# Optimization experiments

Measured on AMD Instinct MI355X. Metric: run time of the kernel, lower is better.

The kernel has to match this reference:

```python
import jax, jax.numpy as jnp
import numpy as np

N_HEAD = 16
D_HEAD = 64
D_MODEL = 1024
D_INNER = 4096
QLEN = 1024
MLEN = 1024
BSZ = 2
LN_EPS = 1e-5


def _layer_norm(x, g, b, eps=LN_EPS):
    mu = jnp.mean(x, axis=-1, keepdims=True)
    var = jnp.var(x, axis=-1, keepdims=True)
    return (x - mu) * jax.lax.rsqrt(var + eps) * g + b


def _rel_shift(x):
    # x: [qlen, rlen, bsz, n_head]
    q, r, b, n = x.shape
    zp = jnp.zeros((q, 1, b, n), x.dtype)
    xp = jnp.concatenate([zp, x], axis=1).reshape(r + 1, q, b, n)
    return xp[1:].reshape(q, r, b, n)


def setup_inputs() -> dict:
    key = jax.random.key(0)
    ks = jax.random.split(key, 12)
    klen = MLEN + QLEN
    w = jax.random.normal(ks[0], (QLEN, BSZ, D_MODEL), jnp.float32)
    r = jax.random.normal(ks[1], (klen, D_MODEL), jnp.float32)
    mems = jax.random.normal(ks[2], (MLEN, BSZ, D_MODEL), jnp.float32)
    # causal mask: query i attends keys j <= i + mlen
    i = jnp.arange(QLEN)[:, None]
    j = jnp.arange(klen)[None, :]
    attn_mask = (j > i + MLEN)[:, :, None]  # [qlen, klen, 1] bool
    s = 0.02
    params = dict(
        qkv_w=jax.random.normal(ks[3], (3 * N_HEAD * D_HEAD, D_MODEL), jnp.float32) * s,
        r_net_w=jax.random.normal(ks[4], (N_HEAD * D_HEAD, D_MODEL), jnp.float32) * s,
        o_w=jax.random.normal(ks[5], (D_MODEL, N_HEAD * D_HEAD), jnp.float32) * s,
        r_r_bias=jax.random.normal(ks[6], (N_HEAD, D_HEAD), jnp.float32) * s,
        r_w_bias=jax.random.normal(ks[7], (N_HEAD, D_HEAD), jnp.float32) * s,
        ln1_g=jnp.ones((D_MODEL,), jnp.float32),
        ln1_b=jnp.zeros((D_MODEL,), jnp.float32),
        ff_w1=jax.random.normal(ks[8], (D_INNER, D_MODEL), jnp.float32) * s,
        ff_b1=jnp.zeros((D_INNER,), jnp.float32),
        ff_w2=jax.random.normal(ks[9], (D_MODEL, D_INNER), jnp.float32) * s,
        ff_b2=jnp.zeros((D_MODEL,), jnp.float32),
        ln2_g=jnp.ones((D_MODEL,), jnp.float32),
        ln2_b=jnp.zeros((D_MODEL,), jnp.float32),
    )
    return dict(w=w, r=r, mems=mems, attn_mask=attn_mask, **params)


def reference(w, r, mems, attn_mask, qkv_w, r_net_w, o_w, r_r_bias, r_w_bias,
              ln1_g, ln1_b, ff_w1, ff_b1, ff_w2, ff_b2, ln2_g, ln2_b):
    qlen, bsz = w.shape[0], w.shape[1]
    scale = 1.0 / (D_HEAD ** 0.5)
    cat = jnp.concatenate([mems, w], axis=0)              # [klen, b, d_model]
    klen = cat.shape[0]
    w_heads = cat @ qkv_w.T                                # [klen, b, 3*n*d]
    wq, wk, wv = jnp.split(w_heads, 3, axis=-1)
    wq = wq[-qlen:]
    r_head_k = (r @ r_net_w.T).reshape(-1, N_HEAD, D_HEAD)  # [rlen, n, d]
    wq = wq.reshape(qlen, bsz, N_HEAD, D_HEAD)
    wk = wk.reshape(klen, bsz, N_HEAD, D_HEAD)
    wv = wv.reshape(klen, bsz, N_HEAD, D_HEAD)
    AC = jnp.einsum('ibnd,jbnd->ijbn', wq + r_w_bias, wk)   # content term
    BD = jnp.einsum('ibnd,jnd->ijbn', wq + r_r_bias, r_head_k)
    BD = _rel_shift(BD)                                     # position term
    attn_score = (AC + BD) * scale
    mask_value = jnp.finfo(attn_score.dtype).min
    attn_score = jnp.where(attn_mask[:, :, :, None], mask_value, attn_score)
    attn_prob = jax.nn.softmax(attn_score, axis=1)
    attn_vec = jnp.einsum('ijbn,jbnd->ibnd', attn_prob, wv)
    attn_vec = attn_vec.reshape(qlen, bsz, N_HEAD * D_HEAD)
    attn_out = attn_vec @ o_w.T
    h = _layer_norm(w + attn_out, ln1_g, ln1_b)             # post-lnorm
    core = jax.nn.relu(h @ ff_w1.T + ff_b1) @ ff_w2.T + ff_b2
    out = _layer_norm(h + core, ln2_g, ln2_b)
    return out
```

## Files before the change

### kernel.cpp

```cpp
#include <hip/hip_runtime.h>
#include <math.h>

#define QLEN 1024
#define MLEN 1024
#define KLEN 2048
#define BSZc 2
#define NH 16
#define DH 64
#define DM 1024
#define DI 4096

typedef unsigned short ushort_t;
typedef __attribute__((ext_vector_type(8))) short short8;
typedef __attribute__((ext_vector_type(4))) float f32x4;

__device__ __forceinline__ ushort_t f2bf(float x) {
    unsigned int u = __float_as_uint(x);
    unsigned int r = (u + 0x7FFFu + ((u >> 16) & 1u)) >> 16;
    return (ushort_t)r;
}

__device__ __forceinline__ void gload_lds16(const ushort_t* g, ushort_t* l) {
    __builtin_amdgcn_global_load_lds(
        (const __attribute__((address_space(1))) unsigned int*)g,
        (__attribute__((address_space(3))) unsigned int*)l,
        16, 0, 0);
}

__device__ __forceinline__ void cast8(const float* s, ushort_t* d, int g) {
    const float4 a = *(const float4*)(s + g * 8);
    const float4 b = *(const float4*)(s + g * 8 + 4);
    short8 o;
    o[0] = (short)f2bf(a.x); o[1] = (short)f2bf(a.y);
    o[2] = (short)f2bf(a.z); o[3] = (short)f2bf(a.w);
    o[4] = (short)f2bf(b.x); o[5] = (short)f2bf(b.y);
    o[6] = (short)f2bf(b.z); o[7] = (short)f2bf(b.w);
    *(short8*)(d + g * 8) = o;
}

__global__ __launch_bounds__(256)
void cast_phase1(const float* __restrict__ qkv_w, const float* __restrict__ rnet_w,
                 const float* __restrict__ mems, const float* __restrict__ w,
                 const float* __restrict__ r,
                 ushort_t* __restrict__ W1, ushort_t* __restrict__ W2,
                 ushort_t* __restrict__ Acat, ushort_t* __restrict__ Rsrc)
{
    int g = blockIdx.x * 256 + threadIdx.x;
    if (g < 393216)            { cast8(qkv_w,  W1,              g); }
    else if (g < 524288)       { cast8(rnet_w, W2,              g - 393216); }
    else if (g < 786432)       { cast8(mems,   Acat,            g - 524288); }
    else if (g < 1048576)      { cast8(w,      Acat + 2097152,  g - 786432); }
    else if (g < 1310720)      { cast8(r,      Rsrc,            g - 1048576); }
}

__global__ __launch_bounds__(256)
void cast_phase2(const float* __restrict__ o_w, const float* __restrict__ ffw1,
                 const float* __restrict__ ffw2,
                 ushort_t* __restrict__ W3, ushort_t* __restrict__ W4,
                 ushort_t* __restrict__ W5)
{
    int g = blockIdx.x * 256 + threadIdx.x;
    if (g < 131072)            { cast8(o_w,  W3, g); }
    else if (g < 655360)       { cast8(ffw1, W4, g - 131072); }
    else if (g < 1179648)      { cast8(ffw2, W5, g - 655360); }
}

template<int EMODE, int ACT, int BN>
__global__ __launch_bounds__(256)
void gemm_mfma(const ushort_t* __restrict__ A, const ushort_t* __restrict__ B,
               const float* __restrict__ bias,
               void* __restrict__ O0, int M, int N, int K)
{
    constexpr int JT = BN / 32;
    __shared__ ushort_t At[128 * 32];
    __shared__ ushort_t Bt[BN * 32];

    const int tid  = threadIdx.x;
    const int lane = tid & 63;
    const int w    = tid >> 6;
    const int lr   = lane & 15;
    const int quad = lane >> 4;
    const int m0   = blockIdx.x * 128;
    const int n0   = blockIdx.y * BN;
    const int wm0  = (w >> 1) * 64;
    const int wn0  = (w & 1) * (BN / 2);

    f32x4 acc[4][JT];
#pragma unroll
    for (int it = 0; it < 4; ++it)
#pragma unroll
        for (int jt = 0; jt < JT; ++jt) acc[it][jt] = (f32x4){0.f, 0.f, 0.f, 0.f};

    const int srow = lane >> 2;
    const int scol = (lane & 3) << 3;
    const ushort_t* Ag = A + (size_t)(m0 + w * 32 + srow) * K + scol;
    ushort_t* lA0 = At + (w * 32) * 32;
    ushort_t* lA1 = At + (w * 32 + 16) * 32;
    const ushort_t* Bg;
    ushort_t *lB0, *lB1 = nullptr;
    if (BN == 128) {
        Bg  = B + (size_t)(n0 + w * 32 + srow) * K + scol;
        lB0 = Bt + (w * 32) * 32;
        lB1 = Bt + (w * 32 + 16) * 32;
    } else {
        Bg  = B + (size_t)(n0 + w * 16 + srow) * K + scol;
        lB0 = Bt + (w * 16) * 32;
    }

    const ushort_t* Ato = At + (wm0 + lr) * 32 + quad * 8;
    const ushort_t* Bto = Bt + (wn0 + lr) * 32 + quad * 8;

    for (int k0 = 0; k0 < K; k0 += 32) {
        __syncthreads();
        gload_lds16(Ag + k0, lA0);
        gload_lds16(Ag + (size_t)16 * K + k0, lA1);
        gload_lds16(Bg + k0, lB0);
        if (BN == 128) gload_lds16(Bg + (size_t)16 * K + k0, lB1);
        __syncthreads();

        short8 af[4], bf[JT];
#pragma unroll
        for (int it = 0; it < 4; ++it)
            af[it] = *(const short8*)(Ato + it * 16 * 32);
#pragma unroll
        for (int jt = 0; jt < JT; ++jt)
            bf[jt] = *(const short8*)(Bto + jt * 16 * 32);
#pragma unroll
        for (int it = 0; it < 4; ++it)
#pragma unroll
            for (int jt = 0; jt < JT; ++jt)
                acc[it][jt] = __builtin_amdgcn_mfma_f32_16x16x32_bf16(
                    af[it], bf[jt], acc[it][jt], 0, 0, 0);
    }

#pragma unroll
    for (int it = 0; it < 4; ++it)
#pragma unroll
        for (int jt = 0; jt < JT; ++jt)
#pragma unroll
            for (int rg = 0; rg < 4; ++rg) {
                const int m = m0 + wm0 + it * 16 + quad * 4 + rg;
                const int n = n0 + wn0 + jt * 16 + lr;
                float v = acc[it][jt][rg];
                if (EMODE == 0) {
                    if (bias) v += bias[n];
                    ((float*)O0)[(size_t)m * N + n] = v;
                } else {
                    v += bias[n];
                    if (ACT == 1) v = fmaxf(v, 0.f);
                    ((ushort_t*)O0)[(size_t)m * N + n] = f2bf(v);
                }
            }
}

__global__ __launch_bounds__(256)
void gemm_qkvr(const ushort_t* __restrict__ Acat, const ushort_t* __restrict__ W1,
               const ushort_t* __restrict__ Rsrc, const ushort_t* __restrict__ W2,
               ushort_t* __restrict__ Qac, ushort_t* __restrict__ Qbd,
               ushort_t* __restrict__ Kbf, ushort_t* __restrict__ Vtb,
               ushort_t* __restrict__ Rh,
               const float* __restrict__ rwb, const float* __restrict__ rrb)
{
    __shared__ ushort_t At[128 * 32];
    __shared__ ushort_t Bt[128 * 32];

    const int bid  = blockIdx.x;
    const bool isr = bid >= 768;
    const ushort_t* A; const ushort_t* B; int m0, n0;
    if (!isr) { A = Acat; B = W1; m0 = (bid & 31) * 128; n0 = (bid >> 5) * 128; }
    else { int t = bid - 768; A = Rsrc; B = W2; m0 = (t & 15) * 128; n0 = (t >> 4) * 128; }
    const int K = 1024;

    const int tid  = threadIdx.x;
    const int lane = tid & 63;
    const int w    = tid >> 6;
    const int lr   = lane & 15;
    const int quad = lane >> 4;
    const int wm0  = (w >> 1) * 64;
    const int wn0  = (w & 1) * 64;

    f32x4 acc[4][4];
#pragma unroll
    for (int it = 0; it < 4; ++it)
#pragma unroll
        for (int jt = 0; jt < 4; ++jt) acc[it][jt] = (f32x4){0.f, 0.f, 0.f, 0.f};

    const int srow = lane >> 2;
    const int scol = (lane & 3) << 3;
    const ushort_t* Ag = A + (size_t)(m0 + w * 32 + srow) * K + scol;
    const ushort_t* Bg = B + (size_t)(n0 + w * 32 + srow) * K + scol;
    ushort_t* lA0 = At + (w * 32) * 32;
    ushort_t* lA1 = At + (w * 32 + 16) * 32;
    ushort_t* lB0 = Bt + (w * 32) * 32;
    ushort_t* lB1 = Bt + (w * 32 + 16) * 32;

    const ushort_t* Ato = At + (wm0 + lr) * 32 + quad * 8;
    const ushort_t* Bto = Bt + (wn0 + lr) * 32 + quad * 8;

    for (int k0 = 0; k0 < K; k0 += 32) {
        __syncthreads();
        gload_lds16(Ag + k0, lA0);
        gload_lds16(Ag + (size_t)16 * K + k0, lA1);
        gload_lds16(Bg + k0, lB0);
        gload_lds16(Bg + (size_t)16 * K + k0, lB1);
        __syncthreads();

        short8 af[4], bf[4];
#pragma unroll
        for (int it = 0; it < 4; ++it)
            af[it] = *(const short8*)(Ato + it * 16 * 32);
#pragma unroll
        for (int jt = 0; jt < 4; ++jt)
            bf[jt] = *(const short8*)(Bto + jt * 16 * 32);
#pragma unroll
        for (int it = 0; it < 4; ++it)
#pragma unroll
            for (int jt = 0; jt < 4; ++jt)
                acc[it][jt] = __builtin_amdgcn_mfma_f32_16x16x32_bf16(
                    af[it], bf[jt], acc[it][jt], 0, 0, 0);
    }

#pragma unroll
    for (int it = 0; it < 4; ++it)
#pragma unroll
        for (int jt = 0; jt < 4; ++jt)
#pragma unroll
            for (int rg = 0; rg < 4; ++rg) {
                const int m = m0 + wm0 + it * 16 + quad * 4 + rg;
                const int n = n0 + wn0 + jt * 16 + lr;
                const float v = acc[it][jt][rg];
                if (!isr) {
                    const int j = m >> 1, b = m & 1;
                    const int part = n >> 10, hh = (n >> 6) & 15, d = n & 63;
                    if (part == 0) {
                        if (j >= MLEN) {
                            const int qi = j - MLEN;
                            const size_t qidx = (((size_t)(b * NH + hh)) * QLEN + qi) * DH + d;
                            Qac[qidx] = f2bf(v + rwb[hh * DH + d]);
                            Qbd[qidx] = f2bf(v + rrb[hh * DH + d]);
                        }
                    } else if (part == 1) {
                        Kbf[(((size_t)(b * NH + hh)) * KLEN + j) * DH + d] = f2bf(v);
                    } else {
                        Vtb[(((size_t)(b * NH + hh)) * DH + d) * KLEN + j] = f2bf(v);
                    }
                } else {
                    const int hh = n >> 6, d = n & 63;
                    Rh[(((size_t)hh) * KLEN + m) * DH + d] = f2bf(v);
                }
            }
}

__global__ __launch_bounds__(256)
void attn_mfma(const ushort_t* __restrict__ Qac, const ushort_t* __restrict__ Qbd,
               const ushort_t* __restrict__ Kb, const ushort_t* __restrict__ Vt,
               const ushort_t* __restrict__ Rb,
               float* __restrict__ Op0, float* __restrict__ Op1,
               float* __restrict__ Mp, float* __restrict__ Lp)
{
    __shared__ ushort_t Kt[64][72];
    __shared__ ushort_t Rt[128][72];
    __shared__ ushort_t Vl[64][72];
    __shared__ float    Bw[4][16][84];

    const int tid  = threadIdx.x;
    const int lane = tid & 63;
    const int w    = tid >> 6;
    const int lr   = lane & 15;
    const int quad = lane >> 4;
    const int qt   = blockIdx.x;
    const int s    = blockIdx.y;
    const int bh   = blockIdx.z;
    const int i0   = qt << 6;
    const int h    = bh & 15;
    const int b    = bh >> 4;

    short8 qaf[2], qbf[2];
    {
        const size_t rowoff = ((size_t)bh * QLEN + i0 + w * 16 + lr) * DH;
#pragma unroll
        for (int kt = 0; kt < 2; ++kt) {
            qaf[kt] = *(const short8*)(Qac + rowoff + kt * 32 + quad * 8);
            qbf[kt] = *(const short8*)(Qbd + rowoff + kt * 32 + quad * 8);
        }
    }

    f32x4 O[4];
#pragma unroll
    for (int nt = 0; nt < 4; ++nt) O[nt] = (f32x4){0.f, 0.f, 0.f, 0.f};
    float m_run = -3.4e38f, l_run = 0.f;

    const int nc  = qt + 17;
    const int stw = 3 - w;
    const float SC = 0.125f * 1.44269504f;
    const ushort_t* Kh = Kb + (size_t)bh * KLEN * DH;
    const ushort_t* Vh = Vt + (size_t)bh * DH * KLEN;
    const ushort_t* Rhp = Rb + (size_t)h * KLEN * DH;

    for (int c = s; c < nc; c += 2) {
        const int j0 = c << 6;
        const int wb = 960 - i0 + j0;
        __syncthreads();
#pragma unroll
        for (int t = 0; t < 2; ++t) {
            int f = tid + (t << 8);
            int row = f >> 3, c8 = (f & 7) << 3;
            *(int4*)&Kt[row][c8] = *(const int4*)(Kh + (size_t)(j0 + row) * DH + c8);
        }
#pragma unroll
        for (int t = 0; t < 2; ++t) {
            int f = tid + (t << 8);
            int d = f >> 3, c8 = (f & 7) << 3;
            *(int4*)&Vl[d][c8] = *(const int4*)(Vh + (size_t)d * KLEN + j0 + c8);
        }
#pragma unroll
        for (int t = 0; t < 4; ++t) {
            int f = tid + (t << 8);
            int rl2 = f >> 3, c8 = (f & 7) << 3;
            int g = wb + rl2;
            int gc = g > (KLEN - 1) ? (KLEN - 1) : g;
            *(int4*)&Rt[rl2][c8] = *(const int4*)(Rhp + (size_t)gc * DH + c8);
        }
        __syncthreads();

#pragma unroll
        for (int ctl = 0; ctl < 5; ++ctl) {
            const int wr = (stw + ctl) * 16 + lr;
            f32x4 z = (f32x4){0.f, 0.f, 0.f, 0.f};
#pragma unroll
            for (int kt = 0; kt < 2; ++kt) {
                short8 rb2 = *(const short8*)&Rt[wr][kt * 32 + quad * 8];
                z = __builtin_amdgcn_mfma_f32_16x16x32_bf16(qbf[kt], rb2, z, 0, 0, 0);
            }
#pragma unroll
            for (int rg = 0; rg < 4; ++rg)
                Bw[w][quad * 4 + rg][ctl * 16 + lr] = z[rg];
        }
#pragma unroll
        for (int ct = 0; ct < 4; ++ct) {
            f32x4 z = (f32x4){0.f, 0.f, 0.f, 0.f};
#pragma unroll
            for (int kt = 0; kt < 2; ++kt) {
                short8 kb2 = *(const short8*)&Kt[ct * 16 + lr][kt * 32 + quad * 8];
                z = __builtin_amdgcn_mfma_f32_16x16x32_bf16(qaf[kt], kb2, z, 0, 0, 0);
            }
#pragma unroll
            for (int rg = 0; rg < 4; ++rg) {
                const int rrow = quad * 4 + rg;
                Bw[w][rrow][ct * 16 + lr + 15 - rrow] += z[rg];
            }
        }

        const int lim = i0 + w * 16 + lr + 1024 - j0;
        float pv[16];
        float mx = -3.4e38f;
#pragma unroll
        for (int kt = 0; kt < 2; ++kt)
#pragma unroll
            for (int t = 0; t < 8; ++t) {
                const int jj = kt * 32 + quad * 8 + t;
                float sv = Bw[w][lr][jj + 15 - lr] * SC;
                sv = (jj > lim) ? -3.4e38f : sv;
                pv[kt * 8 + t] = sv;
                mx = fmaxf(mx, sv);
            }
        mx = fmaxf(mx, __shfl_xor(mx, 16, 64));
        mx = fmaxf(mx, __shfl_xor(mx, 32, 64));
        const float m_new = fmaxf(m_run, mx);
        float ps = 0.f;
        short8 pf[2];
#pragma unroll
        for (int kt = 0; kt < 2; ++kt)
#pragma unroll
            for (int t = 0; t < 8; ++t) {
                const float e = exp2f(pv[kt * 8 + t] - m_new);
                ps += e;
                pf[kt][t] = (short)f2bf(e);
            }
        ps += __shfl_xor(ps, 16, 64);
        ps += __shfl_xor(ps, 32, 64);
        const float alpha = exp2f(m_run - m_new);
        m_run = m_new;
        l_run = l_run * alpha + ps;

        float ar[4];
#pragma unroll
        for (int rg = 0; rg < 4; ++rg)
            ar[rg] = __shfl(alpha, quad * 4 + rg, 64);
#pragma unroll
        for (int nt = 0; nt < 4; ++nt) {
            O[nt][0] *= ar[0]; O[nt][1] *= ar[1];
            O[nt][2] *= ar[2]; O[nt][3] *= ar[3];
        }
#pragma unroll
        for (int kt = 0; kt < 2; ++kt)
#pragma unroll
            for (int nt = 0; nt < 4; ++nt) {
                short8 vb = *(const short8*)&Vl[nt * 16 + lr][kt * 32 + quad * 8];
                O[nt] = __builtin_amdgcn_mfma_f32_16x16x32_bf16(pf[kt], vb, O[nt], 0, 0, 0);
            }
    }

    if (quad == 0) {
        const size_t mi = ((size_t)s * 32 + bh) * QLEN + i0 + w * 16 + lr;
        Mp[mi] = m_run;
        Lp[mi] = l_run;
    }
    float* Op = s ? Op1 : Op0;
#pragma unroll
    for (int nt = 0; nt < 4; ++nt)
#pragma unroll
        for (int rg = 0; rg < 4; ++rg) {
            const int i = i0 + w * 16 + quad * 4 + rg;
            Op[((size_t)i * BSZc + b) * DM + h * DH + nt * 16 + lr] = O[nt][rg];
        }
}

__global__ __launch_bounds__(256)
void attn_merge(const float* __restrict__ O0, const float* __restrict__ O1,
                const float* __restrict__ Mp, const float* __restrict__ Lp,
                ushort_t* __restrict__ AV)
{
    const int row = blockIdx.x;
    const int tid = threadIdx.x;
    const int i = row >> 1, b = row & 1;
    const int h = tid >> 4;
    const int bh = b * NH + h;
    const size_t mi = (size_t)bh * QLEN + i;
    const float m1 = Mp[mi],            l1 = Lp[mi];
    const float m2 = Mp[32 * QLEN + mi], l2 = Lp[32 * QLEN + mi];
    const float M = fmaxf(m1, m2);
    const float a1 = exp2f(m1 - M), a2 = exp2f(m2 - M);
    const float rl = 1.f / (l1 * a1 + l2 * a2);
    const float f1 = a1 * rl, f2 = a2 * rl;
    const float4 o1 = ((const float4*)(O0 + (size_t)row * DM))[tid];
    const float4 o2 = ((const float4*)(O1 + (size_t)row * DM))[tid];
    ushort_t* p = AV + (size_t)row * DM + tid * 4;
    p[0] = f2bf(o1.x * f1 + o2.x * f2);
    p[1] = f2bf(o1.y * f1 + o2.y * f2);
    p[2] = f2bf(o1.z * f1 + o2.z * f2);
    p[3] = f2bf(o1.w * f1 + o2.w * f2);
}

__global__ __launch_bounds__(256)
void add_ln(const float* __restrict__ X, const float* __restrict__ Y,
            const float* __restrict__ gg, const float* __restrict__ bb,
            float* __restrict__ out, ushort_t* __restrict__ outb)
{
    const int row  = blockIdx.x;
    const int tid  = threadIdx.x;
    const int lane = tid & 63;
    const int w    = tid >> 6;
    __shared__ float ssum[4], ssq[4];

    const float4 xv = ((const float4*)(X + (size_t)row * DM))[tid];
    const float4 yv = ((const float4*)(Y + (size_t)row * DM))[tid];
    const float v0 = xv.x + yv.x, v1 = xv.y + yv.y;
    const float v2 = xv.z + yv.z, v3 = xv.w + yv.w;
    float s = v0 + v1 + v2 + v3;
    float q = v0 * v0 + v1 * v1 + v2 * v2 + v3 * v3;
#pragma unroll
    for (int off = 32; off > 0; off >>= 1) {
        s += __shfl_xor(s, off, 64);
        q += __shfl_xor(q, off, 64);
    }
    if (lane == 0) { ssum[w] = s; ssq[w] = q; }
    __syncthreads();
    s = ssum[0] + ssum[1] + ssum[2] + ssum[3];
    q = ssq[0] + ssq[1] + ssq[2] + ssq[3];
    const float mean = s * (1.f / DM);
    const float var  = q * (1.f / DM) - mean * mean;
    const float rs   = rsqrtf(var + 1e-5f);
    const float4 g4 = ((const float4*)gg)[tid];
    const float4 b4 = ((const float4*)bb)[tid];
    float4 ov;
    ov.x = (v0 - mean) * rs * g4.x + b4.x;
    ov.y = (v1 - mean) * rs * g4.y + b4.y;
    ov.z = (v2 - mean) * rs * g4.z + b4.z;
    ov.w = (v3 - mean) * rs * g4.w + b4.w;
    ((float4*)(out + (size_t)row * DM))[tid] = ov;
    if (outb) {
        ushort_t* p = outb + (size_t)row * DM + tid * 4;
        p[0] = f2bf(ov.x); p[1] = f2bf(ov.y);
        p[2] = f2bf(ov.z); p[3] = f2bf(ov.w);
    }
}

extern "C" void kernel_launch(void* const* d_in, const int* in_sizes, int n_in,
                              void* d_out, int out_size, void* d_ws, size_t ws_size,
                              hipStream_t stream)
{
    (void)in_sizes; (void)n_in; (void)out_size; (void)ws_size;
    const float* w      = (const float*)d_in[0];
    const float* r      = (const float*)d_in[1];
    const float* mems   = (const float*)d_in[2];
    const float* qkv_w  = (const float*)d_in[4];
    const float* rnet_w = (const float*)d_in[5];
    const float* o_w    = (const float*)d_in[6];
    const float* r_r_b  = (const float*)d_in[7];
    const float* r_w_b  = (const float*)d_in[8];
    const float* ln1g   = (const float*)d_in[9];
    const float* ln1b   = (const float*)d_in[10];
    const float* ffw1   = (const float*)d_in[11];
    const float* ffb1   = (const float*)d_in[12];
    const float* ffw2   = (const float*)d_in[13];
    const float* ffb2   = (const float*)d_in[14];
    const float* ln2g   = (const float*)d_in[15];
    const float* ln2b   = (const float*)d_in[16];
    float* out = (float*)d_out;

    char* wsb = (char*)d_ws;
    const size_t MB = 1024 * 1024;
    ushort_t* W1    = (ushort_t*)(wsb + 0 * MB);
    ushort_t* W2    = (ushort_t*)(wsb + 6 * MB);
    ushort_t* Acat  = (ushort_t*)(wsb + 8 * MB);
    ushort_t* Rsrc  = (ushort_t*)(wsb + 16 * MB);
    ushort_t* Qac   = (ushort_t*)(wsb + 20 * MB);
    ushort_t* Qbd   = (ushort_t*)(wsb + 24 * MB);
    ushort_t* Kbf   = (ushort_t*)(wsb + 28 * MB);
    ushort_t* Vt    = (ushort_t*)(wsb + 36 * MB);
    ushort_t* Rh    = (ushort_t*)(wsb + 44 * MB);
    float*    Op0   = (float*)(wsb + 48 * MB);
    float*    Op1   = (float*)(wsb + 56 * MB);
    float*    Mp    = (float*)(wsb + 4 * MB);
    float*    Lp    = (float*)(wsb + 4 * MB + 512 * 1024);
    ushort_t* AVec  = (ushort_t*)(wsb + 0 * MB);
    ushort_t* W3    = (ushort_t*)(wsb + 4 * MB);
    float*    AOut  = (float*)(wsb + 8 * MB);
    float*    Hbuf  = (float*)(wsb + 16 * MB);
    ushort_t* Hbf   = (ushort_t*)(wsb + 24 * MB);
    ushort_t* W4    = (ushort_t*)(wsb + 28 * MB);
    ushort_t* FFbf  = (ushort_t*)(wsb + 36 * MB);
    ushort_t* W5    = (ushort_t*)(wsb + 52 * MB);
    float*    Core  = (float*)(wsb + 0 * MB);

    dim3 blk(256);

    cast_phase1<<<dim3(5120), blk, 0, stream>>>(qkv_w, rnet_w, mems, w, r,
                                                W1, W2, Acat, Rsrc);

    gemm_qkvr<<<dim3(896), blk, 0, stream>>>(
        Acat, W1, Rsrc, W2, Qac, Qbd, Kbf, Vt, Rh, r_w_b, r_r_b);

    attn_mfma<<<dim3(16, 2, 32), blk, 0, stream>>>(
        Qac, Qbd, Kbf, Vt, Rh, Op0, Op1, Mp, Lp);

    attn_merge<<<dim3(2048), blk, 0, stream>>>(Op0, Op1, Mp, Lp, AVec);

    cast_phase2<<<dim3(4608), blk, 0, stream>>>(o_w, ffw1, ffw2, W3, W4, W5);

    gemm_mfma<0, 0, 64><<<dim3(16, 16), blk, 0, stream>>>(
        AVec, W3, nullptr, AOut, 2048, 1024, 1024);

    add_ln<<<dim3(2 * QLEN), blk, 0, stream>>>(w, AOut, ln1g, ln1b, Hbuf, Hbf);

    gemm_mfma<3, 1, 128><<<dim3(16, 32), blk, 0, stream>>>(
        Hbf, W4, ffb1, FFbf, 2048, 4096, 1024);

    gemm_mfma<0, 0, 64><<<dim3(16, 16), blk, 0, stream>>>(
        FFbf, W5, ffb2, Core, 2048, 1024, 4096);

    add_ln<<<dim3(2 * QLEN), blk, 0, stream>>>(Hbuf, Core, ln2g, ln2b, out, nullptr);
}
```

Baseline: 440.6 us.

## Split-K the N=1024 GEMMs, widen K step, and read K/V directly in attention

The GEMM kernel now loads a 64-wide K slab per iteration (two 32-wide LDS buffers) so it synchronises half as often. The two N=1024 GEMMs are split along K into two partial outputs, doubling the grid to fill the CUs, and add_ln sums both partials. Attention no longer stages K and V tiles in LDS and reads them straight from global memory into MFMA operands; with less LDS and a launch bound of 4 it aims for higher occupancy. The trade-offs are more global and cache traffic in attention and extra partial-output bandwidth from split-K.

```diff
diff --git a/kernel.cpp b/kernel.cpp
--- a/kernel.cpp
+++ b/kernel.cpp
@@ -65,15 +65,18 @@
     else if (g < 1179648)      { cast8(ffw2, W5, g - 655360); }
 }
 
-template<int EMODE, int ACT, int BN>
+template<int EMODE, int ACT, int BN, int SPLIT>
 __global__ __launch_bounds__(256)
 void gemm_mfma(const ushort_t* __restrict__ A, const ushort_t* __restrict__ B,
                const float* __restrict__ bias,
-               void* __restrict__ O0, int M, int N, int K)
+               void* __restrict__ O0v, void* __restrict__ O1v,
+               int M, int N, int Ks, int lda, int ldb)
 {
     constexpr int JT = BN / 32;
-    __shared__ ushort_t At[128 * 32];
-    __shared__ ushort_t Bt[BN * 32];
+    __shared__ ushort_t At0[128 * 32];
+    __shared__ ushort_t At1[128 * 32];
+    __shared__ ushort_t Bt0[BN * 32];
+    __shared__ ushort_t Bt1[BN * 32];
 
     const int tid  = threadIdx.x;
     const int lane = tid & 63;
@@ -82,6 +85,8 @@
     const int quad = lane >> 4;
     const int m0   = blockIdx.x * 128;
     const int n0   = blockIdx.y * BN;
+    const int z    = (SPLIT > 1) ? (int)blockIdx.z : 0;
+    const int kbase = z * Ks;
     const int wm0  = (w >> 1) * 64;
     const int wn0  = (w & 1) * (BN / 2);
 
@@ -93,38 +98,66 @@
 
     const int srow = lane >> 2;
     const int scol = (lane & 3) << 3;
-    const ushort_t* Ag = A + (size_t)(m0 + w * 32 + srow) * K + scol;
-    ushort_t* lA0 = At + (w * 32) * 32;
-    ushort_t* lA1 = At + (w * 32 + 16) * 32;
+    const ushort_t* Ag = A + (size_t)(m0 + w * 32 + srow) * lda + kbase + scol;
+    ushort_t* a00 = At0 + (w * 32) * 32;
+    ushort_t* a01 = At0 + (w * 32 + 16) * 32;
+    ushort_t* a10 = At1 + (w * 32) * 32;
+    ushort_t* a11 = At1 + (w * 32 + 16) * 32;
     const ushort_t* Bg;
-    ushort_t *lB0, *lB1 = nullptr;
+    ushort_t *b00, *b01 = nullptr, *b10, *b11 = nullptr;
     if (BN == 128) {
-        Bg  = B + (size_t)(n0 + w * 32 + srow) * K + scol;
-        lB0 = Bt + (w * 32) * 32;
-        lB1 = Bt + (w * 32 + 16) * 32;
+        Bg  = B + (size_t)(n0 + w * 32 + srow) * ldb + kbase + scol;
+        b00 = Bt0 + (w * 32) * 32;
+        b01 = Bt0 + (w * 32 + 16) * 32;
+        b10 = Bt1 + (w * 32) * 32;
+        b11 = Bt1 + (w * 32 + 16) * 32;
     } else {
-        Bg  = B + (size_t)(n0 + w * 16 + srow) * K + scol;
-        lB0 = Bt + (w * 16) * 32;
-    }
-
-    const ushort_t* Ato = At + (wm0 + lr) * 32 + quad * 8;
-    const ushort_t* Bto = Bt + (wn0 + lr) * 32 + quad * 8;
-
-    for (int k0 = 0; k0 < K; k0 += 32) {
+        Bg  = B + (size_t)(n0 + w * 16 + srow) * ldb + kbase + scol;
+        b00 = Bt0 + (w * 16) * 32;
+        b10 = Bt1 + (w * 16) * 32;
+    }
+
+    const ushort_t* Ato0 = At0 + (wm0 + lr) * 32 + quad * 8;
+    const ushort_t* Ato1 = At1 + (wm0 + lr) * 32 + quad * 8;
+    const ushort_t* Bto0 = Bt0 + (wn0 + lr) * 32 + quad * 8;
+    const ushort_t* Bto1 = Bt1 + (wn0 + lr) * 32 + quad * 8;
+
+    for (int k0 = 0; k0 < Ks; k0 += 64) {
         __syncthreads();
-        gload_lds16(Ag + k0, lA0);
-        gload_lds16(Ag + (size_t)16 * K + k0, lA1);
-        gload_lds16(Bg + k0, lB0);
-        if (BN == 128) gload_lds16(Bg + (size_t)16 * K + k0, lB1);
+        gload_lds16(Ag + k0, a00);
+        gload_lds16(Ag + (size_t)16 * lda + k0, a01);
+        gload_lds16(Ag + k0 + 32, a10);
+        gload_lds16(Ag + (size_t)16 * lda + k0 + 32, a11);
+        if (BN == 128) {
+            gload_lds16(Bg + k0, b00);
+            gload_lds16(Bg + (size_t)16 * ldb + k0, b01);
+            gload_lds16(Bg + k0 + 32, b10);
+            gload_lds16(Bg + (size_t)16 * ldb + k0 + 32, b11);
+        } else {
+            gload_lds16(Bg + k0, b00);
+            gload_lds16(Bg + k0 + 32, b10);
+        }
         __syncthreads();
 
         short8 af[4], bf[JT];
 #pragma unroll
         for (int it = 0; it < 4; ++it)
-            af[it] = *(const short8*)(Ato + it * 16 * 32);
+            af[it] = *(const short8*)(Ato0 + it * 16 * 32);
 #pragma unroll
         for (int jt = 0; jt < JT; ++jt)
-            bf[jt] = *(const short8*)(Bto + jt * 16 * 32);
+            bf[jt] = *(const short8*)(Bto0 + jt * 16 * 32);
+#pragma unroll
+        for (int it = 0; it < 4; ++it)
+#pragma unroll
+            for (int jt = 0; jt < JT; ++jt)
+                acc[it][jt] = __builtin_amdgcn_mfma_f32_16x16x32_bf16(
+                    af[it], bf[jt], acc[it][jt], 0, 0, 0);
+#pragma unroll
+        for (int it = 0; it < 4; ++it)
+            af[it] = *(const short8*)(Ato1 + it * 16 * 32);
+#pragma unroll
+        for (int jt = 0; jt < JT; ++jt)
+            bf[jt] = *(const short8*)(Bto1 + jt * 16 * 32);
 #pragma unroll
         for (int it = 0; it < 4; ++it)
 #pragma unroll
@@ -143,12 +176,13 @@
                 const int n = n0 + wn0 + jt * 16 + lr;
                 float v = acc[it][jt][rg];
                 if (EMODE == 0) {
-                    if (bias) v += bias[n];
-                    ((float*)O0)[(size_t)m * N + n] = v;
+                    float* dst = (float*)(z ? O1v : O0v);
+                    if (bias && z == 0) v += bias[n];
+                    dst[(size_t)m * N + n] = v;
                 } else {
                     v += bias[n];
                     if (ACT == 1) v = fmaxf(v, 0.f);
-                    ((ushort_t*)O0)[(size_t)m * N + n] = f2bf(v);
+                    ((ushort_t*)O0v)[(size_t)m * N + n] = f2bf(v);
                 }
             }
 }
@@ -251,16 +285,14 @@
             }
 }
 
-__global__ __launch_bounds__(256)
+__global__ __launch_bounds__(256, 4)
 void attn_mfma(const ushort_t* __restrict__ Qac, const ushort_t* __restrict__ Qbd,
                const ushort_t* __restrict__ Kb, const ushort_t* __restrict__ Vt,
                const ushort_t* __restrict__ Rb,
                float* __restrict__ Op0, float* __restrict__ Op1,
                float* __restrict__ Mp, float* __restrict__ Lp)
 {
-    __shared__ ushort_t Kt[64][72];
     __shared__ ushort_t Rt[128][72];
-    __shared__ ushort_t Vl[64][72];
     __shared__ float    Bw[4][16][84];
 
     const int tid  = threadIdx.x;
@@ -302,18 +334,6 @@
         const int wb = 960 - i0 + j0;
         __syncthreads();
 #pragma unroll
-        for (int t = 0; t < 2; ++t) {
-            int f = tid + (t << 8);
-            int row = f >> 3, c8 = (f & 7) << 3;
-            *(int4*)&Kt[row][c8] = *(const int4*)(Kh + (size_t)(j0 + row) * DH + c8);
-        }
-#pragma unroll
-        for (int t = 0; t < 2; ++t) {
-            int f = tid + (t << 8);
-            int d = f >> 3, c8 = (f & 7) << 3;
-            *(int4*)&Vl[d][c8] = *(const int4*)(Vh + (size_t)d * KLEN + j0 + c8);
-        }
-#pragma unroll
         for (int t = 0; t < 4; ++t) {
             int f = tid + (t << 8);
             int rl2 = f >> 3, c8 = (f & 7) << 3;
@@ -341,7 +361,7 @@
             f32x4 z = (f32x4){0.f, 0.f, 0.f, 0.f};
 #pragma unroll
             for (int kt = 0; kt < 2; ++kt) {
-                short8 kb2 = *(const short8*)&Kt[ct * 16 + lr][kt * 32 + quad * 8];
+                short8 kb2 = *(const short8*)(Kh + (size_t)(j0 + ct * 16 + lr) * DH + kt * 32 + quad * 8);
                 z = __builtin_amdgcn_mfma_f32_16x16x32_bf16(qaf[kt], kb2, z, 0, 0, 0);
             }
 #pragma unroll
@@ -396,7 +416,7 @@
         for (int kt = 0; kt < 2; ++kt)
 #pragma unroll
             for (int nt = 0; nt < 4; ++nt) {
-                short8 vb = *(const short8*)&Vl[nt * 16 + lr][kt * 32 + quad * 8];
+                short8 vb = *(const short8*)(Vh + (size_t)(nt * 16 + lr) * KLEN + j0 + kt * 32 + quad * 8);
                 O[nt] = __builtin_amdgcn_mfma_f32_16x16x32_bf16(pf[kt], vb, O[nt], 0, 0, 0);
             }
     }
@@ -427,7 +447,7 @@
     const int h = tid >> 4;
     const int bh = b * NH + h;
     const size_t mi = (size_t)bh * QLEN + i;
-    const float m1 = Mp[mi],            l1 = Lp[mi];
+    const float m1 = Mp[mi],             l1 = Lp[mi];
     const float m2 = Mp[32 * QLEN + mi], l2 = Lp[32 * QLEN + mi];
     const float M = fmaxf(m1, m2);
     const float a1 = exp2f(m1 - M), a2 = exp2f(m2 - M);
@@ -443,7 +463,8 @@
 }
 
 __global__ __launch_bounds__(256)
-void add_ln(const float* __restrict__ X, const float* __restrict__ Y,
+void add_ln(const float* __restrict__ X, const float* __restrict__ Y0,
+            const float* __restrict__ Y1,
             const float* __restrict__ gg, const float* __restrict__ bb,
             float* __restrict__ out, ushort_t* __restrict__ outb)
 {
@@ -454,9 +475,13 @@
     __shared__ float ssum[4], ssq[4];
 
     const float4 xv = ((const float4*)(X + (size_t)row * DM))[tid];
-    const float4 yv = ((const float4*)(Y + (size_t)row * DM))[tid];
-    const float v0 = xv.x + yv.x, v1 = xv.y + yv.y;
-    const float v2 = xv.z + yv.z, v3 = xv.w + yv.w;
+    const float4 yv = ((const float4*)(Y0 + (size_t)row * DM))[tid];
+    float v0 = xv.x + yv.x, v1 = xv.y + yv.y;
+    float v2 = xv.z + yv.z, v3 = xv.w + yv.w;
+    if (Y1) {
+        const float4 zv = ((const float4*)(Y1 + (size_t)row * DM))[tid];
+        v0 += zv.x; v1 += zv.y; v2 += zv.z; v3 += zv.w;
+    }
     float s = v0 + v1 + v2 + v3;
     float q = v0 * v0 + v1 * v1 + v2 * v2 + v3 * v3;
 #pragma unroll
@@ -526,13 +551,15 @@
     float*    Lp    = (float*)(wsb + 4 * MB + 512 * 1024);
     ushort_t* AVec  = (ushort_t*)(wsb + 0 * MB);
     ushort_t* W3    = (ushort_t*)(wsb + 4 * MB);
-    float*    AOut  = (float*)(wsb + 8 * MB);
+    float*    AOut0 = (float*)(wsb + 8 * MB);
+    float*    AOut1 = (float*)(wsb + 44 * MB);
     float*    Hbuf  = (float*)(wsb + 16 * MB);
     ushort_t* Hbf   = (ushort_t*)(wsb + 24 * MB);
     ushort_t* W4    = (ushort_t*)(wsb + 28 * MB);
     ushort_t* FFbf  = (ushort_t*)(wsb + 36 * MB);
     ushort_t* W5    = (ushort_t*)(wsb + 52 * MB);
-    float*    Core  = (float*)(wsb + 0 * MB);
+    float*    Core0 = (float*)(wsb + 0 * MB);
+    float*    Core1 = (float*)(wsb + 8 * MB);
 
     dim3 blk(256);
 
@@ -549,16 +576,16 @@
 
     cast_phase2<<<dim3(4608), blk, 0, stream>>>(o_w, ffw1, ffw2, W3, W4, W5);
 
-    gemm_mfma<0, 0, 64><<<dim3(16, 16), blk, 0, stream>>>(
-        AVec, W3, nullptr, AOut, 2048, 1024, 1024);
-
-    add_ln<<<dim3(2 * QLEN), blk, 0, stream>>>(w, AOut, ln1g, ln1b, Hbuf, Hbf);
-
-    gemm_mfma<3, 1, 128><<<dim3(16, 32), blk, 0, stream>>>(
-        Hbf, W4, ffb1, FFbf, 2048, 4096, 1024);
-
-    gemm_mfma<0, 0, 64><<<dim3(16, 16), blk, 0, stream>>>(
-        FFbf, W5, ffb2, Core, 2048, 1024, 4096);
-
-    add_ln<<<dim3(2 * QLEN), blk, 0, stream>>>(Hbuf, Core, ln2g, ln2b, out, nullptr);
-}
+    gemm_mfma<0, 0, 64, 2><<<dim3(16, 16, 2), blk, 0, stream>>>(
+        AVec, W3, nullptr, AOut0, AOut1, 2048, 1024, 512, 1024, 1024);
+
+    add_ln<<<dim3(2 * QLEN), blk, 0, stream>>>(w, AOut0, AOut1, ln1g, ln1b, Hbuf, Hbf);
+
+    gemm_mfma<3, 1, 128, 1><<<dim3(16, 32), blk, 0, stream>>>(
+        Hbf, W4, ffb1, FFbf, nullptr, 2048, 4096, 1024, 1024, 1024);
+
+    gemm_mfma<0, 0, 64, 2><<<dim3(16, 16, 2), blk, 0, stream>>>(
+        FFbf, W5, ffb2, Core0, Core1, 2048, 1024, 2048, 4096, 4096);
+
+    add_ln<<<dim3(2 * QLEN), blk, 0, stream>>>(Hbuf, Core0, Core1, ln2g, ln2b, out, nullptr);
+}
```

Result: no change. 437.2 us (-0.8%).
